# Kernel optimization log

Measured on AMD Instinct MI355X. Metric: run time of the kernel, lower is better.

Reference implementation:

```python
import jax, jax.numpy as jnp
import numpy as np

DIM = 768
GP_NUM = 49


def setup_inputs() -> dict:
    key = jax.random.key(0)
    ks = jax.random.split(key, 7)
    b, n, d = 8, 2048, DIM
    s = d ** -0.5
    x = jax.random.normal(ks[0], (b, n, d), dtype=jnp.float32)
    W_qkv = jax.random.normal(ks[1], (d, 3 * d), dtype=jnp.float32) * s
    b_qkv = jnp.zeros((3 * d,), dtype=jnp.float32)
    W_proj = jax.random.normal(ks[2], (d, d), dtype=jnp.float32) * s
    b_proj = jnp.zeros((d,), dtype=jnp.float32)
    W_gp = jax.random.normal(ks[3], (d, GP_NUM), dtype=jnp.float32) * s
    alpha = jax.random.normal(ks[4], (), dtype=jnp.float32)
    return {"x": x, "W_qkv": W_qkv, "b_qkv": b_qkv, "W_proj": W_proj,
            "b_proj": b_proj, "W_gp": W_gp, "alpha": alpha}


def reference(x, W_qkv, b_qkv, W_proj, b_proj, W_gp, alpha):
    d = x.shape[-1]
    scale = d ** -0.5
    qkv = x @ W_qkv + b_qkv            # [b, n, 3d]
    q, k, v = jnp.split(qkv, 3, axis=-1)
    # full n x n attention scores
    attn_scores = jnp.einsum('bnd,bmd->bnm', q, k) * scale
    # group affinity: softmax(gelu(v @ W_gp)) then outer product over groups
    gw = jax.nn.softmax(jax.nn.gelu(v @ W_gp, approximate=False), axis=-1)  # [b, n, g]
    group_weight = jnp.einsum('bng,bmg->bnm', gw, gw)  # [b, n, n]
    attn_scores = jax.nn.softmax(attn_scores * group_weight, axis=-1)
    a = jax.nn.sigmoid(alpha)
    attn_weights = (1.0 - a) * attn_scores + a * group_weight
    out = jnp.einsum('bnm,bmd->bnd', attn_weights, v)
    return out @ W_proj + b_proj
```

## Files before the change

### kernel.cpp

```cpp
#include <hip/hip_runtime.h>
#include <hip/hip_bf16.h>
#include <math.h>

#define CB 8
#define CN 2048
#define CD 768
#define CDQKV 2304
#define NG 49
#define SLD 2112

typedef unsigned short ushort_t;
typedef __attribute__((ext_vector_type(8))) short bf16x8;
typedef __attribute__((ext_vector_type(4))) float f32x4;

__device__ __forceinline__ float bf2f(ushort_t u) {
    unsigned int x = ((unsigned int)u) << 16;
    return __builtin_bit_cast(float, x);
}
__device__ __forceinline__ ushort_t f2bf(float f) {
    unsigned int u = __builtin_bit_cast(unsigned int, f);
    u += 0x7fff + ((u >> 16) & 1);
    return (ushort_t)(u >> 16);
}
__device__ __forceinline__ ushort_t f2h(float f) {
    _Float16 h = (_Float16)f;
    return __builtin_bit_cast(ushort_t, h);
}
__device__ __forceinline__ float h2f(ushort_t u) {
    return (float)__builtin_bit_cast(_Float16, u);
}
__device__ __forceinline__ float sigmoidf_(float x) { return 1.f / (1.f + __expf(-x)); }

__device__ __forceinline__ void gload_lds16(const ushort_t* g, ushort_t* l) {
    __builtin_amdgcn_global_load_lds((const __attribute__((address_space(1))) void*)g,
                                     (__attribute__((address_space(3))) void*)l, 16, 0, 0);
}

__global__ void ws_fail_marker(float* out) {
    if (threadIdx.x == 0 && blockIdx.x == 0) out[0] = 31337.0f;
}

__global__ __launch_bounds__(256) void cast_bf16(const float* __restrict__ X,
                                                 ushort_t* __restrict__ XB, int n)
{
    int i = (blockIdx.x * 256 + threadIdx.x) * 8;
    if (i >= n) return;
    float4 a = *(const float4*)(X + i);
    float4 b = *(const float4*)(X + i + 4);
    ushort_t t[8];
    t[0] = f2bf(a.x); t[1] = f2bf(a.y); t[2] = f2bf(a.z); t[3] = f2bf(a.w);
    t[4] = f2bf(b.x); t[5] = f2bf(b.y); t[6] = f2bf(b.z); t[7] = f2bf(b.w);
    *(uint4*)(XB + i) = *(uint4*)t;
}

__global__ __launch_bounds__(256) void wt_kernel(const float* __restrict__ W,
                                                 ushort_t* __restrict__ WT,
                                                 int rows, int cols)
{
    __shared__ ushort_t tile[64][72];
    const int bx = blockIdx.x, by = blockIdx.y;
    const int t = threadIdx.x;
    const int r = t >> 2, cp = (t & 3) * 16;
    const float* src = W + (size_t)(by * 64 + r) * cols + bx * 64 + cp;
    ushort_t tmp[16];
#pragma unroll
    for (int i = 0; i < 16; i += 4) {
        float4 v = *(const float4*)(src + i);
        tmp[i + 0] = f2bf(v.x); tmp[i + 1] = f2bf(v.y);
        tmp[i + 2] = f2bf(v.z); tmp[i + 3] = f2bf(v.w);
    }
    *(uint4*)&tile[r][cp] = *(uint4*)tmp;
    *(uint4*)&tile[r][cp + 8] = *(uint4*)(tmp + 8);
    __syncthreads();
#pragma unroll
    for (int i = 0; i < 16; i++) tmp[i] = tile[cp + i][r];
    ushort_t* dst = WT + (size_t)(bx * 64 + r) * rows + by * 64 + cp;
    *(uint4*)dst = *(uint4*)tmp;
    *(uint4*)(dst + 8) = *(uint4*)(tmp + 8);
}

__global__ __launch_bounds__(256) void wgpt_kernel(const float* __restrict__ Wg,
                                                   ushort_t* __restrict__ WGPT)
{
    int idx = blockIdx.x * 256 + threadIdx.x;
    if (idx >= 64 * CD) return;
    int gg = idx / CD, k = idx % CD;
    WGPT[idx] = (gg < NG) ? f2bf(Wg[(size_t)k * NG + gg]) : (ushort_t)0;
}

#define GEN_STAGE(dstA_, dstB_, kt_, Abase_, Bbase_, lda_, ldb_) do {          \
    _Pragma("unroll")                                                          \
    for (int _p = 0; _p < 4; _p++) {                                           \
        int _idx = _p * 256 + tid;                                             \
        int _row = _idx >> 3;                                                  \
        int _lsl = (_idx & 7) ^ (_row & 7);                                    \
        gload_lds16((Abase_) + (size_t)_row * (lda_) + (size_t)(kt_) * 64 + _lsl * 8, \
                    (dstA_) + _idx * 8);                                       \
        gload_lds16((Bbase_) + (size_t)_row * (ldb_) + (size_t)(kt_) * 64 + _lsl * 8, \
                    (dstB_) + _idx * 8);                                       \
    } } while (0)

#define G_COMPUTE(srcA_, srcB_) do {                                           \
    _Pragma("unroll")                                                          \
    for (int _ks = 0; _ks < 2; _ks++) {                                        \
        bf16x8 _af[4], _bf[4];                                                 \
        _Pragma("unroll")                                                      \
        for (int _f = 0; _f < 4; _f++) {                                       \
            int _ra = wr * 64 + _f * 16 + c;                                   \
            int _pa = (_ks * 4 + g) ^ (_ra & 7);                               \
            _af[_f] = *(const bf16x8*)((srcA_) + _ra * 64 + _pa * 8);          \
            int _rb = wc * 64 + _f * 16 + c;                                   \
            int _pb = (_ks * 4 + g) ^ (_rb & 7);                               \
            _bf[_f] = *(const bf16x8*)((srcB_) + _rb * 64 + _pb * 8);          \
        }                                                                      \
        _Pragma("unroll")                                                      \
        for (int _mf = 0; _mf < 4; _mf++)                                      \
            _Pragma("unroll")                                                  \
            for (int _nf = 0; _nf < 4; _nf++)                                  \
                acc[_mf * 4 + _nf] = __builtin_amdgcn_mfma_f32_16x16x32_bf16(  \
                    _af[_mf], _bf[_nf], acc[_mf * 4 + _nf], 0, 0, 0);          \
    } } while (0)

#define STAGE_A128(dst_, base_, ld_, kt_) do {                                 \
    _Pragma("unroll")                                                          \
    for (int _p = 0; _p < 4; _p++) {                                           \
        int _idx = _p * 256 + tid;                                             \
        int _row = _idx >> 3;                                                  \
        int _lsl = (_idx & 7) ^ (_row & 7);                                    \
        gload_lds16((base_) + (size_t)_row * (ld_) + (size_t)(kt_) * 64 + _lsl * 8, \
                    (dst_) + _idx * 8);                                        \
    } } while (0)

#define STAGE_B64(dst_, base_, ld_, kt_) do {                                  \
    _Pragma("unroll")                                                          \
    for (int _p = 0; _p < 2; _p++) {                                           \
        int _idx = _p * 256 + tid;                                             \
        int _row = _idx >> 3;                                                  \
        int _lsl = (_idx & 7) ^ (_row & 7);                                    \
        gload_lds16((base_) + (size_t)_row * (ld_) + (size_t)(kt_) * 64 + _lsl * 8, \
                    (dst_) + _idx * 8);                                        \
    } } while (0)

#define N64_COMPUTE(srcA_, srcB_) do {                                         \
    _Pragma("unroll")                                                          \
    for (int _ks = 0; _ks < 2; _ks++) {                                        \
        bf16x8 _af[2], _bf[4];                                                 \
        _Pragma("unroll")                                                      \
        for (int _f = 0; _f < 2; _f++) {                                       \
            int _ra = w * 32 + _f * 16 + c;                                    \
            int _pa = (_ks * 4 + g) ^ (_ra & 7);                               \
            _af[_f] = *(const bf16x8*)((srcA_) + _ra * 64 + _pa * 8);          \
        }                                                                      \
        _Pragma("unroll")                                                      \
        for (int _f = 0; _f < 4; _f++) {                                       \
            int _rb = _f * 16 + c;                                             \
            int _pb = (_ks * 4 + g) ^ (_rb & 7);                               \
            _bf[_f] = *(const bf16x8*)((srcB_) + _rb * 64 + _pb * 8);          \
        }                                                                      \
        _Pragma("unroll")                                                      \
        for (int _mf = 0; _mf < 2; _mf++)                                      \
            _Pragma("unroll")                                                  \
            for (int _nf = 0; _nf < 4; _nf++)                                  \
                acc[_mf * 4 + _nf] = __builtin_amdgcn_mfma_f32_16x16x32_bf16(  \
                    _af[_mf], _bf[_nf], acc[_mf * 4 + _nf], 0, 0, 0);          \
    } } while (0)

template <int OUTMODE, int NK, int LDA, int LDB>
__global__ __launch_bounds__(256, 2) void mfma_gemm(
    const ushort_t* __restrict__ Ag, const ushort_t* __restrict__ Bg,
    const float* __restrict__ bias,
    ushort_t* __restrict__ Qd, ushort_t* __restrict__ Kd, ushort_t* __restrict__ Vd,
    ushort_t* __restrict__ OB, float* __restrict__ OF)
{
    __shared__ __align__(16) ushort_t As[2][128 * 64];
    __shared__ __align__(16) ushort_t Bs[2][128 * 64];
    const int tid = threadIdx.x;
    const int lane = tid & 63;
    const int w = tid >> 6;
    const int c = lane & 15, g = lane >> 4;
    const int wr = w >> 1, wc = w & 1;
    const int m0 = blockIdx.x * 128;
    const int n0 = blockIdx.y * 128;
    const int b = blockIdx.z;

    const ushort_t* Ab;
    const ushort_t* Bb;
    if (OUTMODE == 2) {
        Ab = Ag + ((size_t)b * CN + m0) * LDA;
        Bb = Bg + ((size_t)b * CD + n0) * LDB;
    } else {
        Ab = Ag + (size_t)m0 * LDA;
        Bb = Bg + (size_t)n0 * LDB;
    }

    f32x4 acc[16];
#pragma unroll
    for (int i = 0; i < 16; i++) acc[i] = (f32x4){0.f, 0.f, 0.f, 0.f};

    GEN_STAGE(As[0], Bs[0], 0, Ab, Bb, LDA, LDB);
    __syncthreads();
#pragma unroll 1
    for (int kt = 0; kt < NK; kt++) {
        const int cur = kt & 1;
        if (kt < NK - 1) GEN_STAGE(As[cur ^ 1], Bs[cur ^ 1], kt + 1, Ab, Bb, LDA, LDB);
        G_COMPUTE(As[cur], Bs[cur]);
        __syncthreads();
    }

    if (OUTMODE == 0) {
        const int seg = n0 / CD;
        const int nl0 = n0 % CD;
        ushort_t* dst = (seg == 0) ? Qd : (seg == 1) ? Kd : Vd;
#pragma unroll
        for (int nf = 0; nf < 4; nf++) {
            float bv = bias[n0 + wc * 64 + nf * 16 + c];
            int n = nl0 + wc * 64 + nf * 16 + c;
#pragma unroll
            for (int mf = 0; mf < 4; mf++) {
#pragma unroll
                for (int r = 0; r < 4; r++) {
                    int m = m0 + wr * 64 + mf * 16 + g * 4 + r;
                    dst[(size_t)m * CD + n] = f2bf(acc[mf * 4 + nf][r] + bv);
                }
            }
        }
    } else if (OUTMODE == 1) {
#pragma unroll
        for (int nf = 0; nf < 4; nf++) {
            int n = n0 + wc * 64 + nf * 16 + c;
            float bv = bias[n];
#pragma unroll
            for (int mf = 0; mf < 4; mf++) {
#pragma unroll
                for (int r = 0; r < 4; r++) {
                    int m = m0 + wr * 64 + mf * 16 + g * 4 + r;
                    OF[(size_t)m * CD + n] = acc[mf * 4 + nf][r] + bv;
                }
            }
        }
    } else {
        ushort_t* OPb = OB + ((size_t)b * CN + m0) * CD;
#pragma unroll
        for (int nf = 0; nf < 4; nf++) {
            int n = n0 + wc * 64 + nf * 16 + c;
#pragma unroll
            for (int mf = 0; mf < 4; mf++) {
#pragma unroll
                for (int r = 0; r < 4; r++) {
                    int m = wr * 64 + mf * 16 + g * 4 + r;
                    OPb[(size_t)m * CD + n] = f2bf(acc[mf * 4 + nf][r]);
                }
            }
        }
    }
}

__global__ __launch_bounds__(256, 2) void s_gemm(
    const ushort_t* __restrict__ Qb, const ushort_t* __restrict__ Kb,
    const ushort_t* __restrict__ GWP, ushort_t* __restrict__ S)
{
    __shared__ __align__(16) ushort_t As[2][128 * 64];
    __shared__ __align__(16) ushort_t Bs[2][128 * 64];
    const int tid = threadIdx.x;
    const int lane = tid & 63;
    const int w = tid >> 6;
    const int c = lane & 15, g = lane >> 4;
    const int wr = w >> 1, wc = w & 1;
    const int b = blockIdx.z;
    const int m0 = blockIdx.x * 128;
    const int n0 = blockIdx.y * 128;
    const ushort_t* Ab = Qb + ((size_t)b * CN + m0) * CD;
    const ushort_t* Bb = Kb + ((size_t)b * CN + n0) * CD;

    f32x4 acc[16], gacc[16];
#pragma unroll
    for (int i = 0; i < 16; i++) {
        acc[i] = (f32x4){0.f, 0.f, 0.f, 0.f};
        gacc[i] = (f32x4){0.f, 0.f, 0.f, 0.f};
    }

    GEN_STAGE(As[0], Bs[0], 0, Ab, Bb, CD, CD);

    {
        const ushort_t* Gq = GWP + ((size_t)b * CN + m0) * 64;
        const ushort_t* Gk = GWP + ((size_t)b * CN + n0) * 64;
        bf16x8 gqf[2][4], gkf[2][4];
#pragma unroll
        for (int ks = 0; ks < 2; ks++)
#pragma unroll
            for (int f = 0; f < 4; f++) {
                gqf[ks][f] = *(const bf16x8*)(Gq + (size_t)(wr * 64 + f * 16 + c) * 64 + ks * 32 + g * 8);
                gkf[ks][f] = *(const bf16x8*)(Gk + (size_t)(wc * 64 + f * 16 + c) * 64 + ks * 32 + g * 8);
            }
#pragma unroll
        for (int ks = 0; ks < 2; ks++)
#pragma unroll
            for (int mf = 0; mf < 4; mf++)
#pragma unroll
                for (int nf = 0; nf < 4; nf++)
                    gacc[mf * 4 + nf] = __builtin_amdgcn_mfma_f32_16x16x32_bf16(
                        gqf[ks][mf], gkf[ks][nf], gacc[mf * 4 + nf], 0, 0, 0);
    }

    __syncthreads();
#pragma unroll 1
    for (int kt = 0; kt < 12; kt++) {
        const int cur = kt & 1;
        if (kt < 11) GEN_STAGE(As[cur ^ 1], Bs[cur ^ 1], kt + 1, Ab, Bb, CD, CD);
        G_COMPUTE(As[cur], Bs[cur]);
        __syncthreads();
    }

    ushort_t* Sb = S + ((size_t)b * CN + m0) * SLD + n0;
    const float scale = 0.03608439182435161f;
#pragma unroll
    for (int nf = 0; nf < 4; nf++) {
        int n = wc * 64 + nf * 16 + c;
#pragma unroll
        for (int mf = 0; mf < 4; mf++) {
#pragma unroll
            for (int r = 0; r < 4; r++) {
                int m = wr * 64 + mf * 16 + g * 4 + r;
                float z = acc[mf * 4 + nf][r] * scale * gacc[mf * 4 + nf][r];
                Sb[(size_t)m * SLD + n] = f2h(z);
            }
        }
    }
}

__global__ __launch_bounds__(256, 2) void gw_gemm(
    const ushort_t* __restrict__ Vb, const ushort_t* __restrict__ WGPT,
    ushort_t* __restrict__ GWP, ushort_t* __restrict__ GWT)
{
    __shared__ __align__(16) ushort_t As[2][128 * 64];
    __shared__ __align__(16) ushort_t Bs[2][64 * 64];
    const int tid = threadIdx.x;
    const int lane = tid & 63;
    const int w = tid >> 6;
    const int c = lane & 15, g = lane >> 4;
    const int row0 = blockIdx.x * 128;
    const ushort_t* Ab = Vb + (size_t)row0 * CD;

    f32x4 acc[8];
#pragma unroll
    for (int i = 0; i < 8; i++) acc[i] = (f32x4){0.f, 0.f, 0.f, 0.f};

    STAGE_A128(As[0], Ab, CD, 0);
    STAGE_B64(Bs[0], WGPT, CD, 0);
    __syncthreads();
#pragma unroll 1
    for (int kt = 0; kt < 12; kt++) {
        const int cur = kt & 1;
        if (kt < 11) {
            STAGE_A128(As[cur ^ 1], Ab, CD, kt + 1);
            STAGE_B64(Bs[cur ^ 1], WGPT, CD, kt + 1);
        }
        N64_COMPUTE(As[cur], Bs[cur]);
        __syncthreads();
    }

    float gl[2][4][4];
#pragma unroll
    for (int mf = 0; mf < 2; mf++)
#pragma unroll
        for (int nf = 0; nf < 4; nf++) {
            int col = nf * 16 + c;
#pragma unroll
            for (int rr = 0; rr < 4; rr++) {
                float xx = acc[mf * 4 + nf][rr];
                float ge = 0.5f * xx * (1.f + erff(xx * 0.7071067811865475f));
                gl[mf][nf][rr] = (col < NG) ? ge : -1e30f;
            }
        }
#pragma unroll
    for (int mf = 0; mf < 2; mf++) {
#pragma unroll
        for (int rr = 0; rr < 4; rr++) {
            float m = fmaxf(fmaxf(gl[mf][0][rr], gl[mf][1][rr]),
                            fmaxf(gl[mf][2][rr], gl[mf][3][rr]));
#pragma unroll
            for (int s = 1; s < 16; s <<= 1) m = fmaxf(m, __shfl_xor(m, s, 64));
            float ssum = 0.f;
#pragma unroll
            for (int nf = 0; nf < 4; nf++) {
                int col = nf * 16 + c;
                float e = (col < NG) ? __expf(gl[mf][nf][rr] - m) : 0.f;
                gl[mf][nf][rr] = e;
                ssum += e;
            }
#pragma unroll
            for (int s = 1; s < 16; s <<= 1) ssum += __shfl_xor(ssum, s, 64);
            float inv = 1.f / ssum;
            int row = row0 + w * 32 + mf * 16 + g * 4 + rr;
            int bb = row >> 11, nn = row & 2047;
#pragma unroll
            for (int nf = 0; nf < 4; nf++) {
                int col = nf * 16 + c;
                ushort_t wv = f2bf(gl[mf][nf][rr] * inv);
                GWP[(size_t)row * 64 + col] = wv;
                GWT[((size_t)bb * 64 + col) * CN + nn] = wv;
            }
        }
    }
}

__global__ __launch_bounds__(256, 2) void z_gemm(
    ushort_t* __restrict__ VTt, const ushort_t* __restrict__ GWT)
{
    __shared__ __align__(16) ushort_t As[2][128 * 64];
    __shared__ __align__(16) ushort_t Bs[2][64 * 64];
    const int tid = threadIdx.x;
    const int lane = tid & 63;
    const int w = tid >> 6;
    const int c = lane & 15, g = lane >> 4;
    const int b = blockIdx.y;
    const int m0 = blockIdx.x * 128;
    const ushort_t* Ab = VTt + ((size_t)b * CD + m0) * SLD;
    const ushort_t* Bb = GWT + (size_t)b * 64 * CN;

    f32x4 acc[8];
#pragma unroll
    for (int i = 0; i < 8; i++) acc[i] = (f32x4){0.f, 0.f, 0.f, 0.f};

    STAGE_A128(As[0], Ab, SLD, 0);
    STAGE_B64(Bs[0], Bb, CN, 0);
    __syncthreads();
#pragma unroll 1
    for (int kt = 0; kt < 32; kt++) {
        const int cur = kt & 1;
        if (kt < 31) {
            STAGE_A128(As[cur ^ 1], Ab, SLD, kt + 1);
            STAGE_B64(Bs[cur ^ 1], Bb, CN, kt + 1);
        }
        N64_COMPUTE(As[cur], Bs[cur]);
        __syncthreads();
    }

#pragma unroll
    for (int mf = 0; mf < 2; mf++)
#pragma unroll
        for (int nf = 0; nf < 4; nf++) {
            int col = nf * 16 + c;
#pragma unroll
            for (int rr = 0; rr < 4; rr++) {
                int row = m0 + w * 32 + mf * 16 + g * 4 + rr;
                VTt[((size_t)b * CD + row) * SLD + 2048 + col] = f2bf(acc[mf * 4 + nf][rr]);
            }
        }
}

__global__ __launch_bounds__(256) void softmax_rows(ushort_t* __restrict__ SP,
                                                    const ushort_t* __restrict__ GWP,
                                                    const float* __restrict__ alpha_p)
{
    const int lane = threadIdx.x & 63;
    const int row = blockIdx.x * 4 + (threadIdx.x >> 6);
    ushort_t* rp = SP + (size_t)row * SLD;

    float v[32];
    float mx = -1e30f;
#pragma unroll
    for (int ch = 0; ch < 4; ch++) {
        uint4 u = *(const uint4*)(rp + ch * 512 + lane * 8);
        const unsigned int uu[4] = {u.x, u.y, u.z, u.w};
#pragma unroll
        for (int j = 0; j < 4; j++) {
            float a = h2f((ushort_t)(uu[j] & 0xffff));
            float bq = h2f((ushort_t)(uu[j] >> 16));
            v[ch * 8 + j * 2] = a;
            v[ch * 8 + j * 2 + 1] = bq;
            mx = fmaxf(mx, fmaxf(a, bq));
        }
    }
#pragma unroll
    for (int s = 32; s > 0; s >>= 1) mx = fmaxf(mx, __shfl_xor(mx, s, 64));
    float sum = 0.f;
#pragma unroll
    for (int i = 0; i < 32; i++) {
        v[i] = __expf(v[i] - mx);
        sum += v[i];
    }
#pragma unroll
    for (int s = 32; s > 0; s >>= 1) sum += __shfl_xor(sum, s, 64);
    const float aa = sigmoidf_(alpha_p[0]);
    float sc = (1.f - aa) / sum;
#pragma unroll
    for (int ch = 0; ch < 4; ch++) {
        ushort_t t[8];
#pragma unroll
        for (int j = 0; j < 8; j++) t[j] = f2bf(v[ch * 8 + j] * sc);
        *(uint4*)(rp + ch * 512 + lane * 8) = *(uint4*)t;
    }
    if (lane < 8) {
        const ushort_t* gp = GWP + (size_t)row * 64 + lane * 8;
        ushort_t t[8];
#pragma unroll
        for (int j = 0; j < 8; j++) t[j] = f2bf(aa * bf2f(gp[j]));
        *(uint4*)(rp + 2048 + lane * 8) = *(uint4*)t;
    }
}

__global__ __launch_bounds__(256) void vt_transpose(const ushort_t* __restrict__ VB,
                                                    ushort_t* __restrict__ VTt)
{
    __shared__ ushort_t tile[64][72];
    const int bx = blockIdx.x, by = blockIdx.y, b = blockIdx.z;
    const int t = threadIdx.x;
    const int r = t >> 2, cp = (t & 3) * 16;
    const ushort_t* src = VB + ((size_t)b * CN + bx * 64 + r) * CD + by * 64 + cp;
    *(uint4*)&tile[r][cp] = *(const uint4*)src;
    *(uint4*)&tile[r][cp + 8] = *(const uint4*)(src + 8);
    __syncthreads();
    ushort_t tmp[16];
#pragma unroll
    for (int i = 0; i < 16; i++) tmp[i] = tile[cp + i][r];
    ushort_t* dst = VTt + ((size_t)b * CD + by * 64 + r) * SLD + bx * 64 + cp;
    *(uint4*)dst = *(uint4*)tmp;
    *(uint4*)(dst + 8) = *(uint4*)(tmp + 8);
}

extern "C" void kernel_launch(void* const* d_in, const int* in_sizes, int n_in,
                              void* d_out, int out_size, void* d_ws, size_t ws_size,
                              hipStream_t stream) {
    const float* x      = (const float*)d_in[0];
    const float* W_qkv  = (const float*)d_in[1];
    const float* b_qkv  = (const float*)d_in[2];
    const float* W_proj = (const float*)d_in[3];
    const float* b_proj = (const float*)d_in[4];
    const float* W_gp   = (const float*)d_in[5];
    const float* alpha  = (const float*)d_in[6];
    float* out = (float*)d_out;

    const size_t BND    = (size_t)CB * CN * CD;
    const size_t SZ_BF  = BND * 2;
    const size_t SZ_VT  = (size_t)CB * CD * SLD * 2;
    const size_t SZ_WPT = (size_t)CD * CD * 2;
    const size_t SZ_GWP = (size_t)CB * CN * 64 * 2;
    const size_t SZ_GWT = (size_t)CB * 64 * CN * 2;
    const size_t SZ_WGPT= (size_t)64 * CD * 2;
    const size_t SZ_SP  = (size_t)CB * CN * SLD * 2;
    const size_t need = 4 * SZ_BF + SZ_VT + SZ_WPT + SZ_GWP + SZ_GWT + SZ_WGPT + SZ_SP;
    if (ws_size < need) {
        ws_fail_marker<<<1, 1, 0, stream>>>(out);
        return;
    }
    char* p = (char*)d_ws;
    ushort_t* qb   = (ushort_t*)p; p += SZ_BF;
    ushort_t* kb   = (ushort_t*)p; p += SZ_BF;
    ushort_t* vb   = (ushort_t*)p; p += SZ_BF;
    ushort_t* opb  = (ushort_t*)p; p += SZ_BF;
    ushort_t* vtb  = (ushort_t*)p; p += SZ_VT;
    ushort_t* wpt  = (ushort_t*)p; p += SZ_WPT;
    ushort_t* gwp  = (ushort_t*)p; p += SZ_GWP;
    ushort_t* gwt  = (ushort_t*)p; p += SZ_GWT;
    ushort_t* wgpt = (ushort_t*)p; p += SZ_WGPT;
    ushort_t* sp   = (ushort_t*)p; p += SZ_SP;
    ushort_t* xb  = sp;
    ushort_t* wqt = sp + BND;

    cast_bf16<<<dim3((int)(BND / 8 / 256)), 256, 0, stream>>>(x, xb, (int)BND);
    wt_kernel<<<dim3(36, 12), 256, 0, stream>>>(W_qkv, wqt, CD, CDQKV);
    wt_kernel<<<dim3(12, 12), 256, 0, stream>>>(W_proj, wpt, CD, CD);
    wgpt_kernel<<<dim3(192), 256, 0, stream>>>(W_gp, wgpt);
    mfma_gemm<0, 12, CD, CD><<<dim3(128, 18, 1), 256, 0, stream>>>(
        xb, wqt, b_qkv, qb, kb, vb, nullptr, nullptr);
    gw_gemm<<<dim3(128), 256, 0, stream>>>(vb, wgpt, gwp, gwt);
    vt_transpose<<<dim3(32, 12, 8), 256, 0, stream>>>(vb, vtb);
    z_gemm<<<dim3(6, 8), 256, 0, stream>>>(vtb, gwt);
    s_gemm<<<dim3(16, 16, 8), 256, 0, stream>>>(qb, kb, gwp, sp);
    softmax_rows<<<dim3(4096), 256, 0, stream>>>(sp, gwp, alpha);
    mfma_gemm<2, 33, SLD, SLD><<<dim3(16, 6, 8), 256, 0, stream>>>(
        sp, vtb, nullptr, nullptr, nullptr, nullptr, opb, nullptr);
    mfma_gemm<1, 12, CD, CD><<<dim3(128, 6, 1), 256, 0, stream>>>(
        opb, wpt, b_proj, nullptr, nullptr, nullptr, nullptr, out);
}
```

Measured before the change: 364.3 us.

## Rewrite QK^T score GEMM as 256x256 8-wave ping-pong pipelined kernel

Result: no change. 365.0 us (+0.2%).

```diff
diff --git a/kernel.cpp b/kernel.cpp
--- a/kernel.cpp
+++ b/kernel.cpp
@@ -255,75 +255,168 @@
     }
 }
 
-__global__ __launch_bounds__(256, 2) void s_gemm(
+#define SH8(dst_, base_, ld_, rowoff_, kt_) do {                               \
+    _Pragma("unroll")                                                          \
+    for (int _p2 = 0; _p2 < 2; _p2++) {                                        \
+        int _idx = _p2 * 512 + tid;                                            \
+        int _row = _idx >> 3;                                                  \
+        int _lsl = (_idx & 7) ^ (_row & 7);                                    \
+        gload_lds16((base_) + (size_t)((rowoff_) + _row) * (ld_) + (size_t)(kt_) * 64 + _lsl * 8, \
+                    (dst_) + _idx * 8);                                        \
+    } } while (0)
+
+#define RD_A8(SUB) do {                                                        \
+    const ushort_t* _p = &bufA[cur][wr][0];                                    \
+    _Pragma("unroll")                                                          \
+    for (int _ks = 0; _ks < 2; _ks++)                                          \
+        _Pragma("unroll")                                                      \
+        for (int _mf = 0; _mf < 4; _mf++) {                                    \
+            int _lr = ((SUB) * 4 + _mf) * 16 + cc;                             \
+            int _ph = (_ks * 4 + g) ^ (_lr & 7);                               \
+            af[_ks][_mf] = *(const bf16x8*)(_p + _lr * 64 + _ph * 8);          \
+        } } while (0)
+
+#define RD_B8(SUB, DST) do {                                                   \
+    const ushort_t* _p = &bufB[cur][wc >> 1][0];                               \
+    _Pragma("unroll")                                                          \
+    for (int _ks = 0; _ks < 2; _ks++)                                          \
+        _Pragma("unroll")                                                      \
+        for (int _nf = 0; _nf < 2; _nf++) {                                    \
+            int _lr = (wc & 1) * 64 + ((SUB) * 2 + _nf) * 16 + cc;             \
+            int _ph = (_ks * 4 + g) ^ (_lr & 7);                               \
+            DST[_ks][_nf] = *(const bf16x8*)(_p + _lr * 64 + _ph * 8);         \
+        } } while (0)
+
+#define QM8(MH, NH, BREG) do {                                                 \
+    _Pragma("unroll")                                                          \
+    for (int _ks = 0; _ks < 2; _ks++)                                          \
+        _Pragma("unroll")                                                      \
+        for (int _mf = 0; _mf < 4; _mf++)                                      \
+            _Pragma("unroll")                                                  \
+            for (int _nf = 0; _nf < 2; _nf++)                                  \
+                acc[(MH) * 4 + _mf][(NH) * 2 + _nf] =                          \
+                    __builtin_amdgcn_mfma_f32_16x16x32_bf16(                   \
+                        af[_ks][_mf], BREG[_ks][_nf],                          \
+                        acc[(MH) * 4 + _mf][(NH) * 2 + _nf], 0, 0, 0);         \
+    } while (0)
+
+#define PH_SYNC() do {                                                         \
+    __builtin_amdgcn_s_barrier();                                              \
+    asm volatile("s_waitcnt lgkmcnt(0)" ::: "memory");                         \
+    __builtin_amdgcn_sched_barrier(0);                                         \
+    } while (0)
+
+template <int NK, int LDA, int LDB>
+__global__ __launch_bounds__(512, 2) void s_gemm8p(
     const ushort_t* __restrict__ Qb, const ushort_t* __restrict__ Kb,
     const ushort_t* __restrict__ GWP, ushort_t* __restrict__ S)
 {
-    __shared__ __align__(16) ushort_t As[2][128 * 64];
-    __shared__ __align__(16) ushort_t Bs[2][128 * 64];
+    __shared__ __align__(16) ushort_t bufA[2][2][128 * 64];
+    __shared__ __align__(16) ushort_t bufB[2][2][128 * 64];
+
     const int tid = threadIdx.x;
     const int lane = tid & 63;
     const int w = tid >> 6;
-    const int c = lane & 15, g = lane >> 4;
-    const int wr = w >> 1, wc = w & 1;
-    const int b = blockIdx.z;
-    const int m0 = blockIdx.x * 128;
-    const int n0 = blockIdx.y * 128;
-    const ushort_t* Ab = Qb + ((size_t)b * CN + m0) * CD;
-    const ushort_t* Bb = Kb + ((size_t)b * CN + n0) * CD;
-
-    f32x4 acc[16], gacc[16];
-#pragma unroll
-    for (int i = 0; i < 16; i++) {
-        acc[i] = (f32x4){0.f, 0.f, 0.f, 0.f};
-        gacc[i] = (f32x4){0.f, 0.f, 0.f, 0.f};
-    }
-
-    GEN_STAGE(As[0], Bs[0], 0, Ab, Bb, CD, CD);
-
-    {
-        const ushort_t* Gq = GWP + ((size_t)b * CN + m0) * 64;
-        const ushort_t* Gk = GWP + ((size_t)b * CN + n0) * 64;
-        bf16x8 gqf[2][4], gkf[2][4];
+    const int cc = lane & 15, g = lane >> 4;
+    const int wr = w >> 2, wc = w & 3;
+
+    const int per = gridDim.x >> 3;
+    const int idx = (blockIdx.x & 7) * per + (blockIdx.x >> 3);
+    const int bb = idx >> 6;
+    const int m0 = ((idx >> 3) & 7) * 256;
+    const int n0 = (idx & 7) * 256;
+
+    const ushort_t* Ab = Qb + ((size_t)bb * CN + m0) * LDA;
+    const ushort_t* Bb = Kb + ((size_t)bb * CN + n0) * LDB;
+
+    f32x4 acc[8][4];
+#pragma unroll
+    for (int i = 0; i < 8; i++)
+#pragma unroll
+        for (int j = 0; j < 4; j++) acc[i][j] = (f32x4){0.f, 0.f, 0.f, 0.f};
+
+    SH8(&bufA[0][0][0], Ab, LDA, 0, 0);
+    SH8(&bufB[0][0][0], Bb, LDB, 0, 0);
+    SH8(&bufA[0][1][0], Ab, LDA, 128, 0);
+    SH8(&bufB[0][1][0], Bb, LDB, 128, 0);
+    SH8(&bufB[1][0][0], Bb, LDB, 0, 1);
+    SH8(&bufA[1][0][0], Ab, LDA, 0, 1);
+    asm volatile("s_waitcnt vmcnt(4)" ::: "memory");
+    __builtin_amdgcn_s_barrier();
+
+    bf16x8 af[2][4], b0F[2][2], b1F[2][2];
+
+#pragma unroll 1
+    for (int kt = 0; kt < NK; kt++) {
+        const int cur = kt & 1, opp = cur ^ 1;
+        if (kt + 1 < NK) SH8(&bufB[opp][1][0], Bb, LDB, 128, kt + 1);
+        RD_A8(0); RD_B8(0, b0F);
+        PH_SYNC();
+        __builtin_amdgcn_s_setprio(1); QM8(0, 0, b0F); __builtin_amdgcn_s_setprio(0);
+        __builtin_amdgcn_s_barrier();
+        if (kt + 1 < NK) SH8(&bufA[opp][1][0], Ab, LDA, 128, kt + 1);
+        RD_B8(1, b1F);
+        PH_SYNC();
+        __builtin_amdgcn_s_setprio(1); QM8(0, 1, b1F); __builtin_amdgcn_s_setprio(0);
+        __builtin_amdgcn_s_barrier();
+        if (kt + 2 < NK) SH8(&bufB[cur][0][0], Bb, LDB, 0, kt + 2);
+        RD_A8(1);
+        PH_SYNC();
+        __builtin_amdgcn_s_setprio(1); QM8(1, 1, b1F); __builtin_amdgcn_s_setprio(0);
+        __builtin_amdgcn_s_barrier();
+        if (kt + 2 < NK) SH8(&bufA[cur][0][0], Ab, LDA, 0, kt + 2);
+        __builtin_amdgcn_s_setprio(1); QM8(1, 0, b0F); __builtin_amdgcn_s_setprio(0);
+        if (kt < NK - 2) { asm volatile("s_waitcnt vmcnt(4)" ::: "memory"); }
+        else            { asm volatile("s_waitcnt vmcnt(0)" ::: "memory"); }
+        __builtin_amdgcn_s_barrier();
+    }
+
+    const float scale = 0.03608439182435161f;
+    const ushort_t* Gq = GWP + ((size_t)bb * CN + m0) * 64;
+    const ushort_t* Gk = GWP + ((size_t)bb * CN + n0) * 64;
+    ushort_t* Sb = S + ((size_t)bb * CN + m0) * SLD + n0;
+#pragma unroll
+    for (int bh = 0; bh < 2; bh++) {
+        bf16x8 gkf[2][2];
 #pragma unroll
         for (int ks = 0; ks < 2; ks++)
 #pragma unroll
-            for (int f = 0; f < 4; f++) {
-                gqf[ks][f] = *(const bf16x8*)(Gq + (size_t)(wr * 64 + f * 16 + c) * 64 + ks * 32 + g * 8);
-                gkf[ks][f] = *(const bf16x8*)(Gk + (size_t)(wc * 64 + f * 16 + c) * 64 + ks * 32 + g * 8);
-            }
-#pragma unroll
-        for (int ks = 0; ks < 2; ks++)
+            for (int nf = 0; nf < 2; nf++)
+                gkf[ks][nf] = *(const bf16x8*)(
+                    Gk + (size_t)(wc * 64 + (bh * 2 + nf) * 16 + cc) * 64 + ks * 32 + g * 8);
+#pragma unroll
+        for (int ah = 0; ah < 2; ah++) {
+            bf16x8 gqf[2][4];
+#pragma unroll
+            for (int ks = 0; ks < 2; ks++)
+#pragma unroll
+                for (int mf = 0; mf < 4; mf++)
+                    gqf[ks][mf] = *(const bf16x8*)(
+                        Gq + (size_t)(wr * 128 + (ah * 4 + mf) * 16 + cc) * 64 + ks * 32 + g * 8);
+            f32x4 gq[4][2];
 #pragma unroll
             for (int mf = 0; mf < 4; mf++)
 #pragma unroll
-                for (int nf = 0; nf < 4; nf++)
-                    gacc[mf * 4 + nf] = __builtin_amdgcn_mfma_f32_16x16x32_bf16(
-                        gqf[ks][mf], gkf[ks][nf], gacc[mf * 4 + nf], 0, 0, 0);
-    }
-
-    __syncthreads();
-#pragma unroll 1
-    for (int kt = 0; kt < 12; kt++) {
-        const int cur = kt & 1;
-        if (kt < 11) GEN_STAGE(As[cur ^ 1], Bs[cur ^ 1], kt + 1, Ab, Bb, CD, CD);
-        G_COMPUTE(As[cur], Bs[cur]);
-        __syncthreads();
-    }
-
-    ushort_t* Sb = S + ((size_t)b * CN + m0) * SLD + n0;
-    const float scale = 0.03608439182435161f;
-#pragma unroll
-    for (int nf = 0; nf < 4; nf++) {
-        int n = wc * 64 + nf * 16 + c;
-#pragma unroll
-        for (int mf = 0; mf < 4; mf++) {
-#pragma unroll
-            for (int r = 0; r < 4; r++) {
-                int m = wr * 64 + mf * 16 + g * 4 + r;
-                float z = acc[mf * 4 + nf][r] * scale * gacc[mf * 4 + nf][r];
-                Sb[(size_t)m * SLD + n] = f2h(z);
-            }
+                for (int nf = 0; nf < 2; nf++) gq[mf][nf] = (f32x4){0.f, 0.f, 0.f, 0.f};
+#pragma unroll
+            for (int ks = 0; ks < 2; ks++)
+#pragma unroll
+                for (int mf = 0; mf < 4; mf++)
+#pragma unroll
+                    for (int nf = 0; nf < 2; nf++)
+                        gq[mf][nf] = __builtin_amdgcn_mfma_f32_16x16x32_bf16(
+                            gqf[ks][mf], gkf[ks][nf], gq[mf][nf], 0, 0, 0);
+#pragma unroll
+            for (int mf = 0; mf < 4; mf++)
+#pragma unroll
+                for (int nf = 0; nf < 2; nf++)
+#pragma unroll
+                    for (int r = 0; r < 4; r++) {
+                        int m = wr * 128 + (ah * 4 + mf) * 16 + g * 4 + r;
+                        int n = wc * 64 + (bh * 2 + nf) * 16 + cc;
+                        float z = acc[ah * 4 + mf][bh * 2 + nf][r] * scale * gq[mf][nf][r];
+                        Sb[(size_t)m * SLD + n] = f2h(z);
+                    }
         }
     }
 }
@@ -567,7 +660,7 @@
     gw_gemm<<<dim3(128), 256, 0, stream>>>(vb, wgpt, gwp, gwt);
     vt_transpose<<<dim3(32, 12, 8), 256, 0, stream>>>(vb, vtb);
     z_gemm<<<dim3(6, 8), 256, 0, stream>>>(vtb, gwt);
-    s_gemm<<<dim3(16, 16, 8), 256, 0, stream>>>(qb, kb, gwp, sp);
+    s_gemm8p<12, CD, CD><<<dim3(512), 512, 0, stream>>>(qb, kb, gwp, sp);
     softmax_rows<<<dim3(4096), 256, 0, stream>>>(sp, gwp, alpha);
     mfma_gemm<2, 33, SLD, SLD><<<dim3(16, 6, 8), 256, 0, stream>>>(
         sp, vtb, nullptr, nullptr, nullptr, nullptr, opb, nullptr);
```
